# Performance work log

Hardware: AMD Instinct MI355X
Metric: run time of the kernel (lower is better)

## Reference

```python
import jax, jax.numpy as jnp
import numpy as np

C = jnp.complex64
NQ = 4  # qubits per register (module-level `qubits` constant)

_CNOT = jnp.array([[1,0,0,0],[0,1,0,0],[0,0,0,1],[0,0,1,0]], dtype=C)
_X = jnp.array([[0,1],[1,0]], dtype=C)

def _RZ(t):
    e = jnp.exp((-0.5j) * t.astype(C))
    z = jnp.zeros((), C)
    return jnp.stack([jnp.stack([e, z]), jnp.stack([z, jnp.conj(e)])])

def _RX(t):
    c = jnp.cos(0.5 * t).astype(C)
    s = (-1j) * jnp.sin(0.5 * t).astype(C)
    return jnp.stack([jnp.stack([c, s]), jnp.stack([s, c])])

def _CRX(t):
    return jnp.eye(4, dtype=C).at[2:, 2:].set(_RX(t))

def _IXX(t):
    c = jnp.cos(0.5 * t).astype(C)
    s = (-1j) * jnp.sin(0.5 * t).astype(C)
    return c * jnp.eye(4, dtype=C) + s * jnp.fliplr(jnp.eye(4, dtype=C))

def _ap1(psi, U, w):
    psi = jnp.moveaxis(psi, w, 0)
    psi = jnp.tensordot(U, psi, axes=([1], [0]))
    return jnp.moveaxis(psi, 0, w)

def _ap2(psi, U, w1, w2):
    psi = jnp.moveaxis(psi, (w1, w2), (0, 1))
    shp = psi.shape
    psi = (U @ psi.reshape(4, -1)).reshape(shp)
    return jnp.moveaxis(psi, (0, 1), (w1, w2))

def _expZ(psi, w):
    p = psi.real ** 2 + psi.imag ** 2
    p = jnp.moveaxis(p, w, 0).reshape(2, -1).sum(axis=1)
    return p[0] - p[1]

def _expX(psi, w):
    return jnp.real(jnp.vdot(psi, _ap1(psi, _X, w)))

def _init_state(n):
    return jnp.zeros((2,) * n, C).at[(0,) * n].set(1.0 + 0.0j)

def _rot_layer(psi, rot, offset, start):
    for i in range(NQ):
        idx = start + 3 * i
        w = offset + i
        psi = _ap1(psi, _RZ(rot[idx]), w)
        psi = _ap1(psi, _RX(rot[idx + 1]), w)
        psi = _ap1(psi, _RZ(rot[idx + 2]), w)
    return psi

def _two_ring(psi, rot, crx, offset):
    # depth == 2 (24 rot params): one rot layer before entanglers, one after.
    psi = _rot_layer(psi, rot, offset, 0)
    for i in range(NQ):
        psi = _ap2(psi, _CRX(crx[i]), offset + i, offset + (i + 1) % NQ)
    for i in range(NQ):  # len(crx)==2*NQ -> IsingXX ring
        psi = _ap2(psi, _IXX(crx[NQ + i]), offset + i, offset + (i + 1) % NQ)
    psi = _rot_layer(psi, rot, offset, 3 * NQ)
    return psi

def _score_circuit(xq, xk, wq_rot, wq_crx, wk_rot, wk_crx, wc_rot, wc_crx, wc_crx2):
    psi = _init_state(2 * NQ)
    for i in range(NQ):  # AngleEmbedding (default rotation='X')
        psi = _ap1(psi, _RX(xq[i]), i)
    psi = _two_ring(psi, wq_rot, wq_crx, 0)
    for i in range(NQ):
        psi = _ap1(psi, _RX(xk[i]), NQ + i)
    psi = _two_ring(psi, wk_rot, wk_crx, NQ)
    for i in range(NQ):
        psi = _ap2(psi, _CRX(wc_crx[i]), i, i + NQ)
        psi = _ap2(psi, _CRX(wc_crx[i + NQ]), i + NQ, i)
    for i in range(NQ):
        psi = _ap2(psi, _CRX(wc_crx2[i]), i, (i + 1) % NQ + NQ)
    for i in range(NQ):
        psi = _ap2(psi, _CRX(wc_crx2[i + NQ]), i + NQ, (i + 1) % NQ)
    for i in range(NQ):
        psi = _ap2(psi, _CNOT, i, i + NQ)
        psi = _ap2(psi, _CNOT, i + NQ, i)
    psi = _rot_layer(psi, wc_rot, 0, 0)
    z = jnp.stack([_expZ(psi, w) for w in range(NQ)])
    x = jnp.stack([_expX(psi, w) for w in range(NQ)])
    return jnp.concatenate([z, x])

def _value_circuit(xv, amp, wv_rot, wv_crx, gates):
    psi = _init_state(NQ)
    for i in range(NQ):
        psi = _ap1(psi, _RX(xv[i]), i)
    psi = _two_ring(psi, wv_rot, wv_crx, 0)
    for i in range(NQ):
        psi = _ap1(psi, _RX(jnp.tanh(amp[i]) * gates[i]), i)
    for i in range(NQ):
        psi = _ap2(psi, _CNOT, i, (i + 1) % NQ)
    z = jnp.stack([_expZ(psi, w) for w in range(NQ)])
    x = jnp.stack([_expX(psi, w) for w in range(NQ)])
    return jnp.concatenate([z, x])

def setup_inputs() -> dict:
    key = jax.random.key(0)
    ks = jax.random.split(key, 16)
    B, IN = 4096, 96
    hp = np.pi / 2
    return {
        'x_text': jax.random.normal(ks[0], (B, IN), jnp.float32),
        'x_image': jax.random.normal(ks[1], (B, IN), jnp.float32),
        'W_text': jax.random.normal(ks[2], (NQ, IN), jnp.float32) * 0.1,
        'b_text': jnp.zeros((NQ,), jnp.float32),
        'W_image': jax.random.normal(ks[3], (NQ, IN), jnp.float32) * 0.1,
        'b_image': jnp.zeros((NQ,), jnp.float32),
        'weights_q_rot': jax.random.uniform(ks[4], (6 * NQ,), jnp.float32, -hp, hp),
        'weights_q_crx': jax.random.normal(ks[5], (2 * NQ,), jnp.float32) * 0.1,
        'weights_k_rot': jax.random.uniform(ks[6], (6 * NQ,), jnp.float32, -hp, hp),
        'weights_k_crx': jax.random.normal(ks[7], (2 * NQ,), jnp.float32) * 0.1,
        'weights_v_rot': jax.random.uniform(ks[8], (6 * NQ,), jnp.float32, -hp, hp),
        'weights_v_crx': jax.random.normal(ks[9], (2 * NQ,), jnp.float32) * 0.1,
        'weights_cross_rot': jax.random.uniform(ks[10], (3 * NQ,), jnp.float32, -hp, hp),
        'weights_cross_crx': jax.random.normal(ks[11], (2 * NQ,), jnp.float32) * 0.1,
        'weights_cross_crx2': jax.random.normal(ks[12], (2 * NQ,), jnp.float32) * 0.1,
        'score_gates': jnp.full((NQ,), np.pi, jnp.float32),
    }

def reference(x_text, x_image, W_text, b_text, W_image, b_image,
              weights_q_rot, weights_q_crx, weights_k_rot, weights_k_crx,
              weights_v_rot, weights_v_crx, weights_cross_rot,
              weights_cross_crx, weights_cross_crx2, score_gates):
    # anneal alpha = 1.0 and all QAFConfig flags True -> effective params = raw params
    xq = x_text @ W_text.T + b_text   # [B, 4]
    xk = x_image @ W_image.T + b_image
    score = jax.vmap(lambda a, b: _score_circuit(
        a, b, weights_q_rot, weights_q_crx, weights_k_rot, weights_k_crx,
        weights_cross_rot, weights_cross_crx, weights_cross_crx2))(xq, xk)  # [B, 8]
    amp = jnp.sqrt(score[:, :NQ] ** 2 + score[:, NQ:] ** 2)  # [B, 4]
    out = jax.vmap(lambda v, a: _value_circuit(
        v, a, weights_v_rot, weights_v_crx, score_gates))(xk, amp)  # [B, 8]
    return out.astype(jnp.float32)
```

## Files before the change

### kernel.cpp

```cpp
#include <hip/hip_runtime.h>
#include <math.h>

#define DEV __device__ __forceinline__

template<int M>
DEV float lxor(float x) {
    const int i = __builtin_bit_cast(int, x);
    int r;
    if constexpr (M == 1)      r = __builtin_amdgcn_update_dpp(i, i, 0xB1, 0xF, 0xF, false);
    else if constexpr (M == 2) r = __builtin_amdgcn_update_dpp(i, i, 0x4E, 0xF, 0xF, false);
    else if constexpr (M == 3) r = __builtin_amdgcn_update_dpp(i, i, 0x1B, 0xF, 0xF, false);
    else if constexpr (M == 8) r = __builtin_amdgcn_update_dpp(i, i, 0x128, 0xF, 0xF, false);
    else                       r = __builtin_amdgcn_ds_swizzle(i, (M << 10) | 0x1F);
    return __builtin_bit_cast(float, r);
}
template<int M> DEV float2 lxor2(float2 v) {
    return make_float2(lxor<M>(v.x), lxor<M>(v.y));
}
DEV float red16(float x) {
    x += lxor<8>(x); x += lxor<4>(x); x += lxor<2>(x); x += lxor<1>(x);
    return x;
}

template<int RM>
DEV void rgate(float2 (&s)[16], float2 u00, float2 u01) {
#pragma unroll
    for (int r = 0; r < 16; r++) {
        if (r & RM) continue;
        const int r1 = r | RM;
        const float2 a = s[r], b = s[r1];
        s[r]  = make_float2(u00.x*a.x - u00.y*a.y + u01.x*b.x - u01.y*b.y,
                            u00.x*a.y + u00.y*a.x + u01.x*b.y + u01.y*b.x);
        s[r1] = make_float2(u00.x*b.x + u00.y*b.y - u01.x*a.x - u01.y*a.y,
                            u00.x*b.y - u00.y*b.x - u01.x*a.y + u01.y*a.x);
    }
}
template<int RM>
DEV void rgate4(float2 (&s)[16], float4 g) {
    rgate<RM>(s, make_float2(g.x, g.y), make_float2(g.z, g.w));
}

template<int LM>
DEV void lgate(float2 (&s)[16], int l4, float2 u00, float2 u01) {
    const bool hi = (l4 & LM) != 0;
    const float e00x = u00.x, e00y = hi ? -u00.y : u00.y;
    const float e01x = hi ? -u01.x : u01.x, e01y = u01.y;
#pragma unroll
    for (int r = 0; r < 16; r++) {
        const float2 p = lxor2<LM>(s[r]);
        const float2 a = s[r];
        s[r] = make_float2(e00x*a.x - e00y*a.y + e01x*p.x - e01y*p.y,
                           e00x*a.y + e00y*a.x + e01x*p.y + e01y*p.x);
    }
}
template<int LM>
DEV void lgate4(float2 (&s)[16], int l4, float4 g) {
    lgate<LM>(s, l4, make_float2(g.x, g.y), make_float2(g.z, g.w));
}

template<int CM, int TM>
DEV void crx_rr(float2 (&s)[16], float2 cs) {
#pragma unroll
    for (int r = 0; r < 16; r++) {
        if (!(r & CM) || (r & TM)) continue;
        const int r1 = r | TM;
        const float2 a = s[r], b = s[r1];
        s[r]  = make_float2(cs.x*a.x + cs.y*b.y, cs.x*a.y - cs.y*b.x);
        s[r1] = make_float2(cs.x*b.x + cs.y*a.y, cs.x*b.y - cs.y*a.x);
    }
}
template<int CL, int TM>
DEV void crx_lr(float2 (&s)[16], int l4, float2 cs) {
    const bool hi = (l4 & CL) != 0;
    const float c = hi ? cs.x : 1.f, sn = hi ? cs.y : 0.f;
#pragma unroll
    for (int r = 0; r < 16; r++) {
        if (r & TM) continue;
        const int r1 = r | TM;
        const float2 a = s[r], b = s[r1];
        s[r]  = make_float2(c*a.x + sn*b.y, c*a.y - sn*b.x);
        s[r1] = make_float2(c*b.x + sn*a.y, c*b.y - sn*a.x);
    }
}
template<int CM, int LM>
DEV void crx_rl(float2 (&s)[16], float2 cs) {
#pragma unroll
    for (int r = 0; r < 16; r++) {
        if (!(r & CM)) continue;
        const float2 p = lxor2<LM>(s[r]);
        const float2 a = s[r];
        s[r] = make_float2(cs.x*a.x + cs.y*p.y, cs.x*a.y - cs.y*p.x);
    }
}
template<int CL, int LM>
DEV void crx_ll(float2 (&s)[16], int l4, float2 cs) {
    const bool hi = (l4 & CL) != 0;
    const float c = hi ? cs.x : 1.f, sn = hi ? cs.y : 0.f;
#pragma unroll
    for (int r = 0; r < 16; r++) {
        const float2 p = lxor2<LM>(s[r]);
        const float2 a = s[r];
        s[r] = make_float2(c*a.x + sn*p.y, c*a.y - sn*p.x);
    }
}

template<int M2>
DEV void ixx_rr(float2 (&s)[16], float2 cs) {
    constexpr int HB = (M2 & 8) ? 8 : ((M2 & 4) ? 4 : 2);
#pragma unroll
    for (int r = 0; r < 16; r++) {
        if (r & HB) continue;
        const int r1 = r ^ M2;
        const float2 a = s[r], b = s[r1];
        s[r]  = make_float2(cs.x*a.x + cs.y*b.y, cs.x*a.y - cs.y*b.x);
        s[r1] = make_float2(cs.x*b.x + cs.y*a.y, cs.x*b.y - cs.y*a.x);
    }
}
template<int LM2>
DEV void ixx_ll(float2 (&s)[16], float2 cs) {
#pragma unroll
    for (int r = 0; r < 16; r++) {
        const float2 p = lxor2<LM2>(s[r]);
        const float2 a = s[r];
        s[r] = make_float2(cs.x*a.x + cs.y*p.y, cs.x*a.y - cs.y*p.x);
    }
}

template<int CM, int LM>
DEV void cnot_rl(float2 (&s)[16]) {
#pragma unroll
    for (int r = 0; r < 16; r++) {
        if (r & CM) s[r] = lxor2<LM>(s[r]);
    }
}
template<int CL, int TM>
DEV void cnot_lr(float2 (&s)[16], int l4) {
    const bool hi = (l4 & CL) != 0;
#pragma unroll
    for (int r = 0; r < 16; r++) {
        if (r & TM) continue;
        const int r1 = r | TM;
        const float2 a = s[r], b = s[r1];
        s[r]  = hi ? b : a;
        s[r1] = hi ? a : b;
    }
}

template<int RM>
DEV void measZX(const float2 (&s)[16], float& z, float& x) {
    float zz = 0.f, xx = 0.f;
#pragma unroll
    for (int r = 0; r < 16; r++) {
        const float n2 = s[r].x*s[r].x + s[r].y*s[r].y;
        zz += (r & RM) ? -n2 : n2;
        xx += s[r].x*s[r ^ RM].x + s[r].y*s[r ^ RM].y;
    }
    z = zz; x = xx;
}

DEV void fuse_rx(float4 g, float ang, float2& u00, float2& u01) {
    float s_, c_;
    __sincosf(0.5f * ang, &s_, &c_);
    u00 = make_float2(g.x*c_ + g.w*s_, g.y*c_ - g.z*s_);
    u01 = make_float2(g.y*s_ + g.z*c_, -g.x*s_ + g.w*c_);
}

template<int LM>
DEV void vgate(float2& v, int l4, float2 u00, float2 u01) {
    const bool hi = (l4 & LM) != 0;
    const float e00x = u00.x, e00y = hi ? -u00.y : u00.y;
    const float e01x = hi ? -u01.x : u01.x, e01y = u01.y;
    const float2 p = lxor2<LM>(v);
    v = make_float2(e00x*v.x - e00y*v.y + e01x*p.x - e01y*p.y,
                    e00x*v.y + e00y*v.x + e01x*p.y + e01y*p.x);
}
template<int LM>
DEV void vgate4(float2& v, int l4, float4 g) {
    vgate<LM>(v, l4, make_float2(g.x, g.y), make_float2(g.z, g.w));
}
template<int CL, int LM>
DEV void vcrx(float2& v, int l4, float2 cs) {
    const bool hi = (l4 & CL) != 0;
    const float c = hi ? cs.x : 1.f, sn = hi ? cs.y : 0.f;
    const float2 p = lxor2<LM>(v);
    v = make_float2(c*v.x + sn*p.y, c*v.y - sn*p.x);
}
template<int LM2>
DEV void vixx(float2& v, float2 cs) {
    const float2 p = lxor2<LM2>(v);
    v = make_float2(cs.x*v.x + cs.y*p.y, cs.x*v.y - cs.y*p.x);
}
template<int LM>
DEV void vrx(float2& v, float c, float sn) {
    const float2 p = lxor2<LM>(v);
    v = make_float2(c*v.x + sn*p.y, c*v.y - sn*p.x);
}
template<int CL, int LM>
DEV void vcnot(float2& v, int l4) {
    const float2 p = lxor2<LM>(v);
    const bool hi = (l4 & CL) != 0;
    v = hi ? p : v;
}

__global__ __launch_bounds__(256, 1) void qa_kernel(
    const float* __restrict__ x_text, const float* __restrict__ x_image,
    const float* __restrict__ W_text, const float* __restrict__ b_text,
    const float* __restrict__ W_image, const float* __restrict__ b_image,
    const float* __restrict__ wq_rot, const float* __restrict__ wq_crx,
    const float* __restrict__ wk_rot, const float* __restrict__ wk_crx,
    const float* __restrict__ wv_rot, const float* __restrict__ wv_crx,
    const float* __restrict__ wc_rot, const float* __restrict__ wc_crx,
    const float* __restrict__ wc_crx2, const float* __restrict__ gates,
    float* __restrict__ out, int B)
{
    __shared__ float4 sG[28];
    __shared__ float2 sCS[40];
    __shared__ float4 sWT[192];

    const int tid = threadIdx.x;
    if (tid < 192) {
        const float* W = (tid < 96) ? W_text : W_image;
        const int idx = (tid < 96) ? tid : tid - 96;
        sWT[tid] = make_float4(W[idx], W[96 + idx], W[192 + idx], W[288 + idx]);
    }
    if (tid < 28) {
        const float* srcs[7] = {wq_rot, wq_rot + 12, wk_rot, wk_rot + 12,
                                wc_rot, wv_rot, wv_rot + 12};
        const float* p = srcs[tid >> 2] + 3 * (tid & 3);
        const float a = p[0], bb = p[1], c = p[2];
        float sh, ch, sd, cd, sb, cb;
        __sincosf(0.5f * (a + c), &sh, &ch);
        __sincosf(0.5f * (a - c), &sd, &cd);
        __sincosf(0.5f * bb, &sb, &cb);
        sG[tid] = make_float4(cb * ch, -cb * sh, sb * sd, -sb * cd);
    }
    if (tid < 40) {
        const float* srcs[5] = {wq_crx, wk_crx, wc_crx, wc_crx2, wv_crx};
        const float t = srcs[tid >> 3][tid & 7];
        float s_, c_;
        __sincosf(0.5f * t, &s_, &c_);
        sCS[tid] = make_float2(c_, s_);
    }
    __syncthreads();

    const int l16 = tid & 15;
    const int b = blockIdx.x * 16 + (tid >> 4);

    const float* xt = x_text + (size_t)b * 96;
    const float* xi = x_image + (size_t)b * 96;
    float aq[4] = {0.f, 0.f, 0.f, 0.f}, ak[4] = {0.f, 0.f, 0.f, 0.f};
#pragma unroll
    for (int k = 0; k < 6; k++) {
        const int idx = l16 + 16 * k;
        const float vq = xt[idx], vk = xi[idx];
        const float4 wq = sWT[idx], wk = sWT[96 + idx];
        aq[0] += vq * wq.x; aq[1] += vq * wq.y; aq[2] += vq * wq.z; aq[3] += vq * wq.w;
        ak[0] += vk * wk.x; ak[1] += vk * wk.y; ak[2] += vk * wk.z; ak[3] += vk * wk.w;
    }
    float xq[4], xk[4];
#pragma unroll
    for (int j = 0; j < 4; j++) {
        xq[j] = red16(aq[j]) + b_text[j];
        xk[j] = red16(ak[j]) + b_image[j];
    }

    float2 s[16];
#pragma unroll
    for (int r = 0; r < 16; r++) s[r] = make_float2(0.f, 0.f);
    s[0].x = (l16 == 0) ? 1.f : 0.f;

    {
        float2 u00, u01;
        fuse_rx(sG[0], xq[0], u00, u01); rgate<8>(s, u00, u01);
        fuse_rx(sG[1], xq[1], u00, u01); rgate<4>(s, u00, u01);
        fuse_rx(sG[2], xq[2], u00, u01); rgate<2>(s, u00, u01);
        fuse_rx(sG[3], xq[3], u00, u01); rgate<1>(s, u00, u01);
    }
    crx_rr<8, 4>(s, sCS[0]); crx_rr<4, 2>(s, sCS[1]);
    crx_rr<2, 1>(s, sCS[2]); crx_rr<1, 8>(s, sCS[3]);
    ixx_rr<12>(s, sCS[4]); ixx_rr<6>(s, sCS[5]);
    ixx_rr<3>(s, sCS[6]);  ixx_rr<9>(s, sCS[7]);
    rgate4<8>(s, sG[4]); rgate4<4>(s, sG[5]);
    rgate4<2>(s, sG[6]); rgate4<1>(s, sG[7]);

    {
        float2 u00, u01;
        fuse_rx(sG[8],  xk[0], u00, u01); lgate<8>(s, l16, u00, u01);
        fuse_rx(sG[9],  xk[1], u00, u01); lgate<4>(s, l16, u00, u01);
        fuse_rx(sG[10], xk[2], u00, u01); lgate<2>(s, l16, u00, u01);
        fuse_rx(sG[11], xk[3], u00, u01); lgate<1>(s, l16, u00, u01);
    }
    crx_ll<8, 4>(s, l16, sCS[8]);  crx_ll<4, 2>(s, l16, sCS[9]);
    crx_ll<2, 1>(s, l16, sCS[10]); crx_ll<1, 8>(s, l16, sCS[11]);
    ixx_ll<12>(s, sCS[12]); ixx_ll<6>(s, sCS[13]);
    ixx_ll<3>(s, sCS[14]);  ixx_ll<9>(s, sCS[15]);
    lgate4<8>(s, l16, sG[12]); lgate4<4>(s, l16, sG[13]);
    lgate4<2>(s, l16, sG[14]); lgate4<1>(s, l16, sG[15]);

    crx_rl<8, 8>(s, sCS[16]); crx_lr<8, 8>(s, l16, sCS[20]);
    crx_rl<4, 4>(s, sCS[17]); crx_lr<4, 4>(s, l16, sCS[21]);
    crx_rl<2, 2>(s, sCS[18]); crx_lr<2, 2>(s, l16, sCS[22]);
    crx_rl<1, 1>(s, sCS[19]); crx_lr<1, 1>(s, l16, sCS[23]);
    crx_rl<8, 4>(s, sCS[24]); crx_rl<4, 2>(s, sCS[25]);
    crx_rl<2, 1>(s, sCS[26]); crx_rl<1, 8>(s, sCS[27]);
    crx_lr<8, 4>(s, l16, sCS[28]); crx_lr<4, 2>(s, l16, sCS[29]);
    crx_lr<2, 1>(s, l16, sCS[30]); crx_lr<1, 8>(s, l16, sCS[31]);
    cnot_rl<8, 8>(s); cnot_lr<8, 8>(s, l16);
    cnot_rl<4, 4>(s); cnot_lr<4, 4>(s, l16);
    cnot_rl<2, 2>(s); cnot_lr<2, 2>(s, l16);
    cnot_rl<1, 1>(s); cnot_lr<1, 1>(s, l16);
    rgate4<8>(s, sG[16]); rgate4<4>(s, sG[17]);
    rgate4<2>(s, sG[18]); rgate4<1>(s, sG[19]);

    float amp[4];
    {
        float z0, x0, z1, x1, z2, x2, z3, x3;
        measZX<8>(s, z0, x0); measZX<4>(s, z1, x1);
        measZX<2>(s, z2, x2); measZX<1>(s, z3, x3);
        z0 = red16(z0); x0 = red16(x0);
        z1 = red16(z1); x1 = red16(x1);
        z2 = red16(z2); x2 = red16(x2);
        z3 = red16(z3); x3 = red16(x3);
        amp[0] = sqrtf(z0 * z0 + x0 * x0);
        amp[1] = sqrtf(z1 * z1 + x1 * x1);
        amp[2] = sqrtf(z2 * z2 + x2 * x2);
        amp[3] = sqrtf(z3 * z3 + x3 * x3);
    }

    float2 v = make_float2((l16 == 0) ? 1.f : 0.f, 0.f);
    {
        float2 u00, u01;
        fuse_rx(sG[20], xk[0], u00, u01); vgate<8>(v, l16, u00, u01);
        fuse_rx(sG[21], xk[1], u00, u01); vgate<4>(v, l16, u00, u01);
        fuse_rx(sG[22], xk[2], u00, u01); vgate<2>(v, l16, u00, u01);
        fuse_rx(sG[23], xk[3], u00, u01); vgate<1>(v, l16, u00, u01);
    }
    vcrx<8, 4>(v, l16, sCS[32]); vcrx<4, 2>(v, l16, sCS[33]);
    vcrx<2, 1>(v, l16, sCS[34]); vcrx<1, 8>(v, l16, sCS[35]);
    vixx<12>(v, sCS[36]); vixx<6>(v, sCS[37]);
    vixx<3>(v, sCS[38]);  vixx<9>(v, sCS[39]);
    vgate4<8>(v, l16, sG[24]); vgate4<4>(v, l16, sG[25]);
    vgate4<2>(v, l16, sG[26]); vgate4<1>(v, l16, sG[27]);
#pragma unroll
    for (int i = 0; i < 4; i++) {
        const float ang = tanhf(amp[i]) * gates[i];
        float s_, c_;
        __sincosf(0.5f * ang, &s_, &c_);
        if (i == 0) vrx<8>(v, c_, s_);
        if (i == 1) vrx<4>(v, c_, s_);
        if (i == 2) vrx<2>(v, c_, s_);
        if (i == 3) vrx<1>(v, c_, s_);
    }
    vcnot<8, 4>(v, l16); vcnot<4, 2>(v, l16);
    vcnot<2, 1>(v, l16); vcnot<1, 8>(v, l16);

    const float n2 = v.x * v.x + v.y * v.y;
    float oz[4], ox[4];
    {
        const float2 p8 = lxor2<8>(v), p4 = lxor2<4>(v),
                     p2 = lxor2<2>(v), p1 = lxor2<1>(v);
        oz[0] = red16((l16 & 8) ? -n2 : n2);
        oz[1] = red16((l16 & 4) ? -n2 : n2);
        oz[2] = red16((l16 & 2) ? -n2 : n2);
        oz[3] = red16((l16 & 1) ? -n2 : n2);
        ox[0] = red16(v.x * p8.x + v.y * p8.y);
        ox[1] = red16(v.x * p4.x + v.y * p4.y);
        ox[2] = red16(v.x * p2.x + v.y * p2.y);
        ox[3] = red16(v.x * p1.x + v.y * p1.y);
    }
    if (l16 == 0) {
        float4* o = (float4*)(out + (size_t)b * 8);
        o[0] = make_float4(oz[0], oz[1], oz[2], oz[3]);
        o[1] = make_float4(ox[0], ox[1], ox[2], ox[3]);
    }
}

extern "C" void kernel_launch(void* const* d_in, const int* in_sizes, int n_in,
                              void* d_out, int out_size, void* d_ws, size_t ws_size,
                              hipStream_t stream) {
    (void)n_in; (void)out_size; (void)d_ws; (void)ws_size;
    const int B = in_sizes[0] / 96;
    const dim3 grid((B + 15) / 16), block(256);
    hipLaunchKernelGGL(qa_kernel, grid, block, 0, stream,
                       (const float*)d_in[0], (const float*)d_in[1],
                       (const float*)d_in[2], (const float*)d_in[3],
                       (const float*)d_in[4], (const float*)d_in[5],
                       (const float*)d_in[6], (const float*)d_in[7],
                       (const float*)d_in[8], (const float*)d_in[9],
                       (const float*)d_in[10], (const float*)d_in[11],
                       (const float*)d_in[12], (const float*)d_in[13],
                       (const float*)d_in[14], (const float*)d_in[15],
                       (float*)d_out, B);
}
```

Before: 102.5 us.

## Simulate Q and K registers separately and fold final rotations into measurement

The Q and K circuits act on disjoint qubits before any cross entanglement, so each register is now evolved as its own 16-amplitude vector, one amplitude per lane, instead of as a 256-amplitude product state in every lane. The two are combined into the joint state by an outer product through shared memory. The final cross rotation layer is folded into precomputed measurement coefficients, so it no longer updates the state. The value circuit's early gates are interleaved with the Q/K work for ILP, and tanhf is replaced by an exp-based formula. This adds shared-memory traffic and changes the floating-point rounding order.

```diff
diff --git a/kernel.cpp b/kernel.cpp
--- a/kernel.cpp
+++ b/kernel.cpp
@@ -22,56 +22,56 @@
     return x;
 }
 
-template<int RM>
-DEV void rgate(float2 (&s)[16], float2 u00, float2 u01) {
-#pragma unroll
-    for (int r = 0; r < 16; r++) {
-        if (r & RM) continue;
-        const int r1 = r | RM;
-        const float2 a = s[r], b = s[r1];
-        s[r]  = make_float2(u00.x*a.x - u00.y*a.y + u01.x*b.x - u01.y*b.y,
-                            u00.x*a.y + u00.y*a.x + u01.x*b.y + u01.y*b.x);
-        s[r1] = make_float2(u00.x*b.x + u00.y*b.y - u01.x*a.x - u01.y*a.y,
-                            u00.x*b.y - u00.y*b.x - u01.x*a.y + u01.y*a.x);
-    }
-}
-template<int RM>
-DEV void rgate4(float2 (&s)[16], float4 g) {
-    rgate<RM>(s, make_float2(g.x, g.y), make_float2(g.z, g.w));
-}
-
 template<int LM>
-DEV void lgate(float2 (&s)[16], int l4, float2 u00, float2 u01) {
-    const bool hi = (l4 & LM) != 0;
+DEV void sgate(float2& v, int l16, float2 u00, float2 u01) {
+    const bool hi = (l16 & LM) != 0;
     const float e00x = u00.x, e00y = hi ? -u00.y : u00.y;
     const float e01x = hi ? -u01.x : u01.x, e01y = u01.y;
-#pragma unroll
-    for (int r = 0; r < 16; r++) {
+    const float2 p = lxor2<LM>(v);
+    v = make_float2(e00x*v.x - e00y*v.y + e01x*p.x - e01y*p.y,
+                    e00x*v.y + e00y*v.x + e01x*p.y + e01y*p.x);
+}
+template<int LM>
+DEV void sgate4(float2& v, int l16, float4 g) {
+    sgate<LM>(v, l16, make_float2(g.x, g.y), make_float2(g.z, g.w));
+}
+template<int CL, int LM>
+DEV void scrx(float2& v, int l16, float2 cs) {
+    const bool hi = (l16 & CL) != 0;
+    const float c = hi ? cs.x : 1.f, sn = hi ? cs.y : 0.f;
+    const float2 p = lxor2<LM>(v);
+    v = make_float2(c*v.x + sn*p.y, c*v.y - sn*p.x);
+}
+template<int LM2>
+DEV void sixx(float2& v, float2 cs) {
+    const float2 p = lxor2<LM2>(v);
+    v = make_float2(cs.x*v.x + cs.y*p.y, cs.x*v.y - cs.y*p.x);
+}
+template<int LM>
+DEV void srx(float2& v, float c, float sn) {
+    const float2 p = lxor2<LM>(v);
+    v = make_float2(c*v.x + sn*p.y, c*v.y - sn*p.x);
+}
+template<int CL, int LM>
+DEV void scnot(float2& v, int l16) {
+    const float2 p = lxor2<LM>(v);
+    const bool hi = (l16 & CL) != 0;
+    v = hi ? p : v;
+}
+
+template<int CM, int LM>
+DEV void crx_rl(float2 (&s)[16], float2 cs) {
+#pragma unroll
+    for (int r = 0; r < 16; r++) {
+        if (!(r & CM)) continue;
         const float2 p = lxor2<LM>(s[r]);
         const float2 a = s[r];
-        s[r] = make_float2(e00x*a.x - e00y*a.y + e01x*p.x - e01y*p.y,
-                           e00x*a.y + e00y*a.x + e01x*p.y + e01y*p.x);
-    }
-}
-template<int LM>
-DEV void lgate4(float2 (&s)[16], int l4, float4 g) {
-    lgate<LM>(s, l4, make_float2(g.x, g.y), make_float2(g.z, g.w));
-}
-
-template<int CM, int TM>
-DEV void crx_rr(float2 (&s)[16], float2 cs) {
-#pragma unroll
-    for (int r = 0; r < 16; r++) {
-        if (!(r & CM) || (r & TM)) continue;
-        const int r1 = r | TM;
-        const float2 a = s[r], b = s[r1];
-        s[r]  = make_float2(cs.x*a.x + cs.y*b.y, cs.x*a.y - cs.y*b.x);
-        s[r1] = make_float2(cs.x*b.x + cs.y*a.y, cs.x*b.y - cs.y*a.x);
+        s[r] = make_float2(cs.x*a.x + cs.y*p.y, cs.x*a.y - cs.y*p.x);
     }
 }
 template<int CL, int TM>
-DEV void crx_lr(float2 (&s)[16], int l4, float2 cs) {
-    const bool hi = (l4 & CL) != 0;
+DEV void crx_lr(float2 (&s)[16], int l16, float2 cs) {
+    const bool hi = (l16 & CL) != 0;
     const float c = hi ? cs.x : 1.f, sn = hi ? cs.y : 0.f;
 #pragma unroll
     for (int r = 0; r < 16; r++) {
@@ -83,50 +83,6 @@
     }
 }
 template<int CM, int LM>
-DEV void crx_rl(float2 (&s)[16], float2 cs) {
-#pragma unroll
-    for (int r = 0; r < 16; r++) {
-        if (!(r & CM)) continue;
-        const float2 p = lxor2<LM>(s[r]);
-        const float2 a = s[r];
-        s[r] = make_float2(cs.x*a.x + cs.y*p.y, cs.x*a.y - cs.y*p.x);
-    }
-}
-template<int CL, int LM>
-DEV void crx_ll(float2 (&s)[16], int l4, float2 cs) {
-    const bool hi = (l4 & CL) != 0;
-    const float c = hi ? cs.x : 1.f, sn = hi ? cs.y : 0.f;
-#pragma unroll
-    for (int r = 0; r < 16; r++) {
-        const float2 p = lxor2<LM>(s[r]);
-        const float2 a = s[r];
-        s[r] = make_float2(c*a.x + sn*p.y, c*a.y - sn*p.x);
-    }
-}
-
-template<int M2>
-DEV void ixx_rr(float2 (&s)[16], float2 cs) {
-    constexpr int HB = (M2 & 8) ? 8 : ((M2 & 4) ? 4 : 2);
-#pragma unroll
-    for (int r = 0; r < 16; r++) {
-        if (r & HB) continue;
-        const int r1 = r ^ M2;
-        const float2 a = s[r], b = s[r1];
-        s[r]  = make_float2(cs.x*a.x + cs.y*b.y, cs.x*a.y - cs.y*b.x);
-        s[r1] = make_float2(cs.x*b.x + cs.y*a.y, cs.x*b.y - cs.y*a.x);
-    }
-}
-template<int LM2>
-DEV void ixx_ll(float2 (&s)[16], float2 cs) {
-#pragma unroll
-    for (int r = 0; r < 16; r++) {
-        const float2 p = lxor2<LM2>(s[r]);
-        const float2 a = s[r];
-        s[r] = make_float2(cs.x*a.x + cs.y*p.y, cs.x*a.y - cs.y*p.x);
-    }
-}
-
-template<int CM, int LM>
 DEV void cnot_rl(float2 (&s)[16]) {
 #pragma unroll
     for (int r = 0; r < 16; r++) {
@@ -134,8 +90,8 @@
     }
 }
 template<int CL, int TM>
-DEV void cnot_lr(float2 (&s)[16], int l4) {
-    const bool hi = (l4 & CL) != 0;
+DEV void cnot_lr(float2 (&s)[16], int l16) {
+    const bool hi = (l16 & CL) != 0;
 #pragma unroll
     for (int r = 0; r < 16; r++) {
         if (r & TM) continue;
@@ -147,13 +103,18 @@
 }
 
 template<int RM>
-DEV void measZX(const float2 (&s)[16], float& z, float& x) {
+DEV void measU(const float2 (&s)[16], const float (&n2)[16],
+               float4 mz, float2 bx, float& z, float& x) {
     float zz = 0.f, xx = 0.f;
 #pragma unroll
     for (int r = 0; r < 16; r++) {
-        const float n2 = s[r].x*s[r].x + s[r].y*s[r].y;
-        zz += (r & RM) ? -n2 : n2;
-        xx += s[r].x*s[r ^ RM].x + s[r].y*s[r ^ RM].y;
+        if (r & RM) continue;
+        const int r1 = r | RM;
+        const float nd  = n2[r] - n2[r1];
+        const float dre = s[r].x*s[r1].x + s[r].y*s[r1].y;
+        const float dim = s[r].x*s[r1].y - s[r].y*s[r1].x;
+        zz += mz.x*nd + mz.y*dre - mz.z*dim;
+        xx += mz.w*nd + bx.x*dre - bx.y*dim;
     }
     z = zz; x = xx;
 }
@@ -163,43 +124,6 @@
     __sincosf(0.5f * ang, &s_, &c_);
     u00 = make_float2(g.x*c_ + g.w*s_, g.y*c_ - g.z*s_);
     u01 = make_float2(g.y*s_ + g.z*c_, -g.x*s_ + g.w*c_);
-}
-
-template<int LM>
-DEV void vgate(float2& v, int l4, float2 u00, float2 u01) {
-    const bool hi = (l4 & LM) != 0;
-    const float e00x = u00.x, e00y = hi ? -u00.y : u00.y;
-    const float e01x = hi ? -u01.x : u01.x, e01y = u01.y;
-    const float2 p = lxor2<LM>(v);
-    v = make_float2(e00x*v.x - e00y*v.y + e01x*p.x - e01y*p.y,
-                    e00x*v.y + e00y*v.x + e01x*p.y + e01y*p.x);
-}
-template<int LM>
-DEV void vgate4(float2& v, int l4, float4 g) {
-    vgate<LM>(v, l4, make_float2(g.x, g.y), make_float2(g.z, g.w));
-}
-template<int CL, int LM>
-DEV void vcrx(float2& v, int l4, float2 cs) {
-    const bool hi = (l4 & CL) != 0;
-    const float c = hi ? cs.x : 1.f, sn = hi ? cs.y : 0.f;
-    const float2 p = lxor2<LM>(v);
-    v = make_float2(c*v.x + sn*p.y, c*v.y - sn*p.x);
-}
-template<int LM2>
-DEV void vixx(float2& v, float2 cs) {
-    const float2 p = lxor2<LM2>(v);
-    v = make_float2(cs.x*v.x + cs.y*p.y, cs.x*v.y - cs.y*p.x);
-}
-template<int LM>
-DEV void vrx(float2& v, float c, float sn) {
-    const float2 p = lxor2<LM>(v);
-    v = make_float2(c*v.x + sn*p.y, c*v.y - sn*p.x);
-}
-template<int CL, int LM>
-DEV void vcnot(float2& v, int l4) {
-    const float2 p = lxor2<LM>(v);
-    const bool hi = (l4 & CL) != 0;
-    v = hi ? p : v;
 }
 
 __global__ __launch_bounds__(256, 1) void qa_kernel(
@@ -216,6 +140,9 @@
     __shared__ float4 sG[28];
     __shared__ float2 sCS[40];
     __shared__ float4 sWT[192];
+    __shared__ float4 sMZ[4];
+    __shared__ float2 sBX[4];
+    __shared__ __align__(16) float2 sQ[16][18];
 
     const int tid = threadIdx.x;
     if (tid < 192) {
@@ -232,7 +159,20 @@
         __sincosf(0.5f * (a + c), &sh, &ch);
         __sincosf(0.5f * (a - c), &sd, &cd);
         __sincosf(0.5f * bb, &sb, &cb);
-        sG[tid] = make_float4(cb * ch, -cb * sh, sb * sd, -sb * cd);
+        const float4 g = make_float4(cb * ch, -cb * sh, sb * sd, -sb * cd);
+        sG[tid] = g;
+        if (tid >= 16 && tid < 20) {
+            const int w = tid - 16;
+            const float2 u00 = make_float2(g.x, g.y), u01 = make_float2(g.z, g.w);
+            const float az = u00.x*u00.x + u00.y*u00.y - u01.x*u01.x - u01.y*u01.y;
+            sMZ[w] = make_float4(az,
+                                 4.f*(u00.x*u01.x + u00.y*u01.y),
+                                 4.f*(u00.x*u01.y - u00.y*u01.x),
+                                 -2.f*(u00.x*u01.x - u00.y*u01.y));
+            sBX[w] = make_float2(
+                2.f*(u00.x*u00.x - u00.y*u00.y - u01.x*u01.x + u01.y*u01.y),
+                -4.f*(u00.x*u00.y + u01.x*u01.y));
+        }
     }
     if (tid < 40) {
         const float* srcs[5] = {wq_crx, wk_crx, wc_crx, wc_crx2, wv_crx};
@@ -244,14 +184,15 @@
     __syncthreads();
 
     const int l16 = tid & 15;
-    const int b = blockIdx.x * 16 + (tid >> 4);
+    const int elem = tid >> 4;
+    const int b = blockIdx.x * 16 + elem;
 
     const float* xt = x_text + (size_t)b * 96;
     const float* xi = x_image + (size_t)b * 96;
     float aq[4] = {0.f, 0.f, 0.f, 0.f}, ak[4] = {0.f, 0.f, 0.f, 0.f};
 #pragma unroll
-    for (int k = 0; k < 6; k++) {
-        const int idx = l16 + 16 * k;
+    for (int kk = 0; kk < 6; kk++) {
+        const int idx = l16 + 16 * kk;
         const float vq = xt[idx], vk = xi[idx];
         const float4 wq = sWT[idx], wk = sWT[96 + idx];
         aq[0] += vq * wq.x; aq[1] += vq * wq.y; aq[2] += vq * wq.z; aq[3] += vq * wq.w;
@@ -264,38 +205,45 @@
         xk[j] = red16(ak[j]) + b_image[j];
     }
 
-    float2 s[16];
-#pragma unroll
-    for (int r = 0; r < 16; r++) s[r] = make_float2(0.f, 0.f);
-    s[0].x = (l16 == 0) ? 1.f : 0.f;
-
+    float2 q  = make_float2((l16 == 0) ? 1.f : 0.f, 0.f);
+    float2 k  = q, vv = q;
     {
         float2 u00, u01;
-        fuse_rx(sG[0], xq[0], u00, u01); rgate<8>(s, u00, u01);
-        fuse_rx(sG[1], xq[1], u00, u01); rgate<4>(s, u00, u01);
-        fuse_rx(sG[2], xq[2], u00, u01); rgate<2>(s, u00, u01);
-        fuse_rx(sG[3], xq[3], u00, u01); rgate<1>(s, u00, u01);
-    }
-    crx_rr<8, 4>(s, sCS[0]); crx_rr<4, 2>(s, sCS[1]);
-    crx_rr<2, 1>(s, sCS[2]); crx_rr<1, 8>(s, sCS[3]);
-    ixx_rr<12>(s, sCS[4]); ixx_rr<6>(s, sCS[5]);
-    ixx_rr<3>(s, sCS[6]);  ixx_rr<9>(s, sCS[7]);
-    rgate4<8>(s, sG[4]); rgate4<4>(s, sG[5]);
-    rgate4<2>(s, sG[6]); rgate4<1>(s, sG[7]);
-
-    {
-        float2 u00, u01;
-        fuse_rx(sG[8],  xk[0], u00, u01); lgate<8>(s, l16, u00, u01);
-        fuse_rx(sG[9],  xk[1], u00, u01); lgate<4>(s, l16, u00, u01);
-        fuse_rx(sG[10], xk[2], u00, u01); lgate<2>(s, l16, u00, u01);
-        fuse_rx(sG[11], xk[3], u00, u01); lgate<1>(s, l16, u00, u01);
-    }
-    crx_ll<8, 4>(s, l16, sCS[8]);  crx_ll<4, 2>(s, l16, sCS[9]);
-    crx_ll<2, 1>(s, l16, sCS[10]); crx_ll<1, 8>(s, l16, sCS[11]);
-    ixx_ll<12>(s, sCS[12]); ixx_ll<6>(s, sCS[13]);
-    ixx_ll<3>(s, sCS[14]);  ixx_ll<9>(s, sCS[15]);
-    lgate4<8>(s, l16, sG[12]); lgate4<4>(s, l16, sG[13]);
-    lgate4<2>(s, l16, sG[14]); lgate4<1>(s, l16, sG[15]);
+        fuse_rx(sG[0],  xq[0], u00, u01); sgate<8>(q,  l16, u00, u01);
+        fuse_rx(sG[8],  xk[0], u00, u01); sgate<8>(k,  l16, u00, u01);
+        fuse_rx(sG[20], xk[0], u00, u01); sgate<8>(vv, l16, u00, u01);
+        fuse_rx(sG[1],  xq[1], u00, u01); sgate<4>(q,  l16, u00, u01);
+        fuse_rx(sG[9],  xk[1], u00, u01); sgate<4>(k,  l16, u00, u01);
+        fuse_rx(sG[21], xk[1], u00, u01); sgate<4>(vv, l16, u00, u01);
+        fuse_rx(sG[2],  xq[2], u00, u01); sgate<2>(q,  l16, u00, u01);
+        fuse_rx(sG[10], xk[2], u00, u01); sgate<2>(k,  l16, u00, u01);
+        fuse_rx(sG[22], xk[2], u00, u01); sgate<2>(vv, l16, u00, u01);
+        fuse_rx(sG[3],  xq[3], u00, u01); sgate<1>(q,  l16, u00, u01);
+        fuse_rx(sG[11], xk[3], u00, u01); sgate<1>(k,  l16, u00, u01);
+        fuse_rx(sG[23], xk[3], u00, u01); sgate<1>(vv, l16, u00, u01);
+    }
+    scrx<8, 4>(q, l16, sCS[0]);  scrx<8, 4>(k, l16, sCS[8]);  scrx<8, 4>(vv, l16, sCS[32]);
+    scrx<4, 2>(q, l16, sCS[1]);  scrx<4, 2>(k, l16, sCS[9]);  scrx<4, 2>(vv, l16, sCS[33]);
+    scrx<2, 1>(q, l16, sCS[2]);  scrx<2, 1>(k, l16, sCS[10]); scrx<2, 1>(vv, l16, sCS[34]);
+    scrx<1, 8>(q, l16, sCS[3]);  scrx<1, 8>(k, l16, sCS[11]); scrx<1, 8>(vv, l16, sCS[35]);
+    sixx<12>(q, sCS[4]);  sixx<12>(k, sCS[12]); sixx<12>(vv, sCS[36]);
+    sixx<6>(q, sCS[5]);   sixx<6>(k, sCS[13]);  sixx<6>(vv, sCS[37]);
+    sixx<3>(q, sCS[6]);   sixx<3>(k, sCS[14]);  sixx<3>(vv, sCS[38]);
+    sixx<9>(q, sCS[7]);   sixx<9>(k, sCS[15]);  sixx<9>(vv, sCS[39]);
+    sgate4<8>(q, l16, sG[4]);  sgate4<8>(k, l16, sG[12]);  sgate4<8>(vv, l16, sG[24]);
+    sgate4<4>(q, l16, sG[5]);  sgate4<4>(k, l16, sG[13]);  sgate4<4>(vv, l16, sG[25]);
+    sgate4<2>(q, l16, sG[6]);  sgate4<2>(k, l16, sG[14]);  sgate4<2>(vv, l16, sG[26]);
+    sgate4<1>(q, l16, sG[7]);  sgate4<1>(k, l16, sG[15]);  sgate4<1>(vv, l16, sG[27]);
+
+    sQ[elem][l16] = q;
+    const float4* qrow = reinterpret_cast<const float4*>(&sQ[elem][0]);
+    float2 s[16];
+#pragma unroll
+    for (int j = 0; j < 8; j++) {
+        const float4 t = qrow[j];
+        s[2*j]   = make_float2(t.x*k.x - t.y*k.y, t.x*k.y + t.y*k.x);
+        s[2*j+1] = make_float2(t.z*k.x - t.w*k.y, t.z*k.y + t.w*k.x);
+    }
 
     crx_rl<8, 8>(s, sCS[16]); crx_lr<8, 8>(s, l16, sCS[20]);
     crx_rl<4, 4>(s, sCS[17]); crx_lr<4, 4>(s, l16, sCS[21]);
@@ -309,64 +257,55 @@
     cnot_rl<4, 4>(s); cnot_lr<4, 4>(s, l16);
     cnot_rl<2, 2>(s); cnot_lr<2, 2>(s, l16);
     cnot_rl<1, 1>(s); cnot_lr<1, 1>(s, l16);
-    rgate4<8>(s, sG[16]); rgate4<4>(s, sG[17]);
-    rgate4<2>(s, sG[18]); rgate4<1>(s, sG[19]);
-
+
+    float n2[16];
+#pragma unroll
+    for (int r = 0; r < 16; r++) n2[r] = s[r].x*s[r].x + s[r].y*s[r].y;
     float amp[4];
     {
         float z0, x0, z1, x1, z2, x2, z3, x3;
-        measZX<8>(s, z0, x0); measZX<4>(s, z1, x1);
-        measZX<2>(s, z2, x2); measZX<1>(s, z3, x3);
+        measU<8>(s, n2, sMZ[0], sBX[0], z0, x0);
+        measU<4>(s, n2, sMZ[1], sBX[1], z1, x1);
+        measU<2>(s, n2, sMZ[2], sBX[2], z2, x2);
+        measU<1>(s, n2, sMZ[3], sBX[3], z3, x3);
         z0 = red16(z0); x0 = red16(x0);
         z1 = red16(z1); x1 = red16(x1);
         z2 = red16(z2); x2 = red16(x2);
         z3 = red16(z3); x3 = red16(x3);
-        amp[0] = sqrtf(z0 * z0 + x0 * x0);
-        amp[1] = sqrtf(z1 * z1 + x1 * x1);
-        amp[2] = sqrtf(z2 * z2 + x2 * x2);
-        amp[3] = sqrtf(z3 * z3 + x3 * x3);
-    }
-
-    float2 v = make_float2((l16 == 0) ? 1.f : 0.f, 0.f);
-    {
-        float2 u00, u01;
-        fuse_rx(sG[20], xk[0], u00, u01); vgate<8>(v, l16, u00, u01);
-        fuse_rx(sG[21], xk[1], u00, u01); vgate<4>(v, l16, u00, u01);
-        fuse_rx(sG[22], xk[2], u00, u01); vgate<2>(v, l16, u00, u01);
-        fuse_rx(sG[23], xk[3], u00, u01); vgate<1>(v, l16, u00, u01);
-    }
-    vcrx<8, 4>(v, l16, sCS[32]); vcrx<4, 2>(v, l16, sCS[33]);
-    vcrx<2, 1>(v, l16, sCS[34]); vcrx<1, 8>(v, l16, sCS[35]);
-    vixx<12>(v, sCS[36]); vixx<6>(v, sCS[37]);
-    vixx<3>(v, sCS[38]);  vixx<9>(v, sCS[39]);
-    vgate4<8>(v, l16, sG[24]); vgate4<4>(v, l16, sG[25]);
-    vgate4<2>(v, l16, sG[26]); vgate4<1>(v, l16, sG[27]);
+        amp[0] = sqrtf(z0*z0 + x0*x0);
+        amp[1] = sqrtf(z1*z1 + x1*x1);
+        amp[2] = sqrtf(z2*z2 + x2*x2);
+        amp[3] = sqrtf(z3*z3 + x3*x3);
+    }
+
 #pragma unroll
     for (int i = 0; i < 4; i++) {
-        const float ang = tanhf(amp[i]) * gates[i];
+        const float e = __expf(2.f * amp[i]);
+        const float th = 1.f - 2.f / (e + 1.f);
+        const float ang = th * gates[i];
         float s_, c_;
         __sincosf(0.5f * ang, &s_, &c_);
-        if (i == 0) vrx<8>(v, c_, s_);
-        if (i == 1) vrx<4>(v, c_, s_);
-        if (i == 2) vrx<2>(v, c_, s_);
-        if (i == 3) vrx<1>(v, c_, s_);
-    }
-    vcnot<8, 4>(v, l16); vcnot<4, 2>(v, l16);
-    vcnot<2, 1>(v, l16); vcnot<1, 8>(v, l16);
-
-    const float n2 = v.x * v.x + v.y * v.y;
+        if (i == 0) srx<8>(vv, c_, s_);
+        if (i == 1) srx<4>(vv, c_, s_);
+        if (i == 2) srx<2>(vv, c_, s_);
+        if (i == 3) srx<1>(vv, c_, s_);
+    }
+    scnot<8, 4>(vv, l16); scnot<4, 2>(vv, l16);
+    scnot<2, 1>(vv, l16); scnot<1, 8>(vv, l16);
+
+    const float vn2 = vv.x*vv.x + vv.y*vv.y;
     float oz[4], ox[4];
     {
-        const float2 p8 = lxor2<8>(v), p4 = lxor2<4>(v),
-                     p2 = lxor2<2>(v), p1 = lxor2<1>(v);
-        oz[0] = red16((l16 & 8) ? -n2 : n2);
-        oz[1] = red16((l16 & 4) ? -n2 : n2);
-        oz[2] = red16((l16 & 2) ? -n2 : n2);
-        oz[3] = red16((l16 & 1) ? -n2 : n2);
-        ox[0] = red16(v.x * p8.x + v.y * p8.y);
-        ox[1] = red16(v.x * p4.x + v.y * p4.y);
-        ox[2] = red16(v.x * p2.x + v.y * p2.y);
-        ox[3] = red16(v.x * p1.x + v.y * p1.y);
+        const float2 p8 = lxor2<8>(vv), p4 = lxor2<4>(vv),
+                     p2 = lxor2<2>(vv), p1 = lxor2<1>(vv);
+        oz[0] = red16((l16 & 8) ? -vn2 : vn2);
+        oz[1] = red16((l16 & 4) ? -vn2 : vn2);
+        oz[2] = red16((l16 & 2) ? -vn2 : vn2);
+        oz[3] = red16((l16 & 1) ? -vn2 : vn2);
+        ox[0] = red16(vv.x*p8.x + vv.y*p8.y);
+        ox[1] = red16(vv.x*p4.x + vv.y*p4.y);
+        ox[2] = red16(vv.x*p2.x + vv.y*p2.y);
+        ox[3] = red16(vv.x*p1.x + vv.y*p1.y);
     }
     if (l16 == 0) {
         float4* o = (float4*)(out + (size_t)b * 8);
```

Result: faster. 93.28 us (-9.0%).
